# Optimization experiments

Measured on AMD Instinct MI355X. Metric: run time of the kernel, lower is better.

## Reference

```python
import jax, jax.numpy as jnp
import numpy as np

BETA = 0.9
TH = 1.0
SLOPE = 25.0  # fast-sigmoid surrogate slope (spike_grad_slope)

@jax.custom_vjp
def spike_fn(m):
    # Heaviside on (mem - threshold)
    return (m > 0).astype(m.dtype)

def _spike_fwd(m):
    return spike_fn(m), m

def _spike_bwd(m, g):
    # fast-sigmoid surrogate gradient: 1 / (slope*|m| + 1)^2
    return (g / (SLOPE * jnp.abs(m) + 1.0) ** 2,)

spike_fn.defvjp(_spike_fwd, _spike_bwd)


def setup_inputs() -> dict:
    key = jax.random.key(0)
    k1, k2, k3 = jax.random.split(key, 3)
    T, B, I, H, O = 128, 8192, 2, 256, 2
    x = jax.random.normal(k1, (T, B, I), dtype=jnp.float32)
    # xavier_uniform with gain=1: limit = sqrt(6/(fan_in+fan_out))
    lim1 = float(np.sqrt(6.0 / (I + H)))
    lim2 = float(np.sqrt(6.0 / (H + O)))
    W1 = jax.random.uniform(k2, (H, I), jnp.float32, -lim1, lim1)
    W2 = jax.random.uniform(k3, (O, H), jnp.float32, -lim2, lim2)
    return {"x": x, "W1": W1, "W2": W2}


def reference(x, W1, W2):
    # Precompute all per-step input currents in one GEMM: [T,B,H]
    cur = jnp.einsum('tbi,hi->tbh', x, W1)
    B, H = cur.shape[1], cur.shape[2]
    mem0 = jnp.zeros((B, H), cur.dtype)

    def step(mem, c):
        # snntorch Leaky (reset_mechanism='subtract'):
        # reset based on PREVIOUS mem's spike, then leaky integrate, then fire
        reset = spike_fn(mem - TH)
        mem_new = BETA * mem + c - reset * TH
        spk = spike_fn(mem_new - TH)
        # original code detaches mem between steps (1-step truncated BPTT)
        return jax.lax.stop_gradient(mem_new), spk

    _, spk_rec = jax.lax.scan(step, mem0, cur)  # spk_rec: [T,B,H]
    spk_avg = spk_rec[-10:].mean(0)             # [B,H]
    out = jnp.einsum('bh,oh->bo', spk_avg, W2)  # [B,O]
    return out
```

## Files before the change

### kernel.cpp

```cpp
#include <hip/hip_runtime.h>


#define T_STEPS 128
#define BATCH   8192
#define HID     256
#define TAIL    10
#define RH      8
#define NP      (RH/2)
#define LB      64
#define NWAVE   4
#define HG      8
#define NBG     (BATCH / LB)
#define PF      8

typedef float f32x2 __attribute__((ext_vector_type(2)));

#define PK_MUL(d, a, b) asm("v_pk_mul_f32 %0, %1, %2" : "=v"(d) : "v"(a), "v"(b))
#define PK_ADD(d, a, b) asm("v_pk_add_f32 %0, %1, %2" : "=v"(d) : "v"(a), "v"(b))

__global__ __launch_bounds__(256) void snn_scan(const float* __restrict__ x,
                                                const float* __restrict__ W1,
                                                const float* __restrict__ W2,
                                                float2* __restrict__ partial) {
    const int tid   = threadIdx.x;
    const int lane  = tid & 63;
    const int wave  = tid >> 6;
    const int bg    = blockIdx.x & (NBG - 1);
    const int hg    = blockIdx.x >> 7;
    const int b     = bg * LB + lane;
    const int hbase = hg * (NWAVE * RH) + wave * RH;

    f32x2 w0p[NP], w1p[NP];
#pragma unroll
    for (int p = 0; p < NP; ++p) {
        w0p[p].x = W1[2 * (hbase + 2 * p)];
        w0p[p].y = W1[2 * (hbase + 2 * p + 1)];
        w1p[p].x = W1[2 * (hbase + 2 * p) + 1];
        w1p[p].y = W1[2 * (hbase + 2 * p + 1) + 1];
    }

    const float2* xp = (const float2*)x;

    f32x2 mem[NP], spkn[NP], cnt[NP];
#pragma unroll
    for (int p = 0; p < NP; ++p) {
        mem[p]  = f32x2{0.0f, 0.0f};
        spkn[p] = f32x2{0.0f, 0.0f};
        cnt[p]  = f32x2{0.0f, 0.0f};
    }

    const f32x2 k09 = {0.9f, 0.9f};

#define LOADX(t) xp[(size_t)(t) * BATCH + b]

#define STEPP(p)                                              \
    {                                                         \
        f32x2 t0, t1, cc, m1, m2;                             \
        PK_MUL(t0, xaa, w0p[p]);                              \
        PK_MUL(t1, xcc, w1p[p]);                              \
        PK_ADD(cc, t0, t1);                                   \
        PK_MUL(m1, k09, mem[p]);                              \
        PK_ADD(m2, m1, cc);                                   \
        PK_ADD(mem[p], m2, spkn[p]);                          \
        spkn[p].x = (mem[p].x > 1.0f) ? -1.0f : 0.0f;         \
        spkn[p].y = (mem[p].y > 1.0f) ? -1.0f : 0.0f;         \
    }

    float2 buf[PF];
#pragma unroll
    for (int j = 0; j < PF; ++j) buf[j] = LOADX(j);

    for (int tb = 0; tb < T_STEPS - 2 * PF; tb += PF) {
#pragma unroll
        for (int j = 0; j < PF; ++j) {
            const float2 xv = buf[j];
            buf[j] = LOADX(tb + PF + j);
            const f32x2 xaa = {xv.x, xv.x};
            const f32x2 xcc = {xv.y, xv.y};
#pragma unroll
            for (int p = 0; p < NP; ++p) STEPP(p)
        }
    }

#pragma unroll
    for (int j = 0; j < PF; ++j) {
        const float2 xv = buf[j];
        buf[j] = LOADX(T_STEPS - PF + j);
        const f32x2 xaa = {xv.x, xv.x};
        const f32x2 xcc = {xv.y, xv.y};
#pragma unroll
        for (int p = 0; p < NP; ++p) {
            STEPP(p)
            if (j >= PF - 2) PK_ADD(cnt[p], cnt[p], spkn[p]);
        }
    }
#pragma unroll
    for (int j = 0; j < PF; ++j) {
        const float2 xv = buf[j];
        const f32x2 xaa = {xv.x, xv.x};
        const f32x2 xcc = {xv.y, xv.y};
#pragma unroll
        for (int p = 0; p < NP; ++p) {
            STEPP(p)
            PK_ADD(cnt[p], cnt[p], spkn[p]);
        }
    }
#undef STEPP
#undef LOADX

    float p0 = 0.0f, p1 = 0.0f;
#pragma unroll
    for (int p = 0; p < NP; ++p) {
        const float a0 = cnt[p].x / -10.0f;
        p0 = __fadd_rn(p0, __fmul_rn(a0, W2[hbase + 2 * p]));
        p1 = __fadd_rn(p1, __fmul_rn(a0, W2[HID + hbase + 2 * p]));
        const float a1 = cnt[p].y / -10.0f;
        p0 = __fadd_rn(p0, __fmul_rn(a1, W2[hbase + 2 * p + 1]));
        p1 = __fadd_rn(p1, __fmul_rn(a1, W2[HID + hbase + 2 * p + 1]));
    }

    __shared__ float2 red[NWAVE][LB];
    red[wave][lane] = make_float2(p0, p1);
    __syncthreads();
    if (wave == 0) {
        const float2 a0 = red[0][lane], a1 = red[1][lane];
        const float2 a2 = red[2][lane], a3 = red[3][lane];
        float2 s;
        s.x = __fadd_rn(__fadd_rn(a0.x, a1.x), __fadd_rn(a2.x, a3.x));
        s.y = __fadd_rn(__fadd_rn(a0.y, a1.y), __fadd_rn(a2.y, a3.y));
        partial[(size_t)hg * BATCH + b] = s;
    }
}

__global__ __launch_bounds__(256) void snn_reduce(const float2* __restrict__ partial,
                                                  float2* __restrict__ out) {
    const int b = blockIdx.x * 256 + threadIdx.x;
    float sx = 0.0f, sy = 0.0f;
#pragma unroll
    for (int hg = 0; hg < HG; ++hg) {
        const float2 p = partial[(size_t)hg * BATCH + b];
        sx = __fadd_rn(sx, p.x);
        sy = __fadd_rn(sy, p.y);
    }
    out[b] = make_float2(sx, sy);
}

extern "C" void kernel_launch(void* const* d_in, const int* in_sizes, int n_in,
                              void* d_out, int out_size, void* d_ws, size_t ws_size,
                              hipStream_t stream) {
    const float* x  = (const float*)d_in[0];
    const float* W1 = (const float*)d_in[1];
    const float* W2 = (const float*)d_in[2];
    float2* out     = (float2*)d_out;
    float2* partial = (float2*)d_ws;

    snn_scan<<<NBG * HG, 256, 0, stream>>>(x, W1, W2, partial);
    snn_reduce<<<BATCH / 256, 256, 0, stream>>>(partial, out);
}
```

Baseline: 103.0 us.

## Fuse cross-block reduction into scan kernel and restructure input-current packed math

Removes the separate reduce kernel launch. The last block of each batch group to finish, detected by a global atomic counter, sums the partials and writes the output. The counter is reset afterwards. Separately, the per-step current computation now multiplies the raw (x0,x1) pair by packed (w0,w1) weights and adds the halves with scalar adds, instead of broadcasting x components. This drops the broadcast moves but changes the instruction mix, and it adds fences and an atomic per block.

```diff
diff --git a/kernel.cpp b/kernel.cpp
--- a/kernel.cpp
+++ b/kernel.cpp
@@ -18,10 +18,13 @@
 #define PK_MUL(d, a, b) asm("v_pk_mul_f32 %0, %1, %2" : "=v"(d) : "v"(a), "v"(b))
 #define PK_ADD(d, a, b) asm("v_pk_add_f32 %0, %1, %2" : "=v"(d) : "v"(a), "v"(b))
 
+__device__ unsigned int bg_done[NBG];
+
 __global__ __launch_bounds__(256) void snn_scan(const float* __restrict__ x,
                                                 const float* __restrict__ W1,
                                                 const float* __restrict__ W2,
-                                                float2* __restrict__ partial) {
+                                                float2* __restrict__ partial,
+                                                float2* __restrict__ out) {
     const int tid   = threadIdx.x;
     const int lane  = tid & 63;
     const int wave  = tid >> 6;
@@ -30,16 +33,12 @@
     const int b     = bg * LB + lane;
     const int hbase = hg * (NWAVE * RH) + wave * RH;
 
-    f32x2 w0p[NP], w1p[NP];
+    f32x2 w01[RH];
+    const f32x2* w1v = (const f32x2*)W1;
 #pragma unroll
-    for (int p = 0; p < NP; ++p) {
-        w0p[p].x = W1[2 * (hbase + 2 * p)];
-        w0p[p].y = W1[2 * (hbase + 2 * p + 1)];
-        w1p[p].x = W1[2 * (hbase + 2 * p) + 1];
-        w1p[p].y = W1[2 * (hbase + 2 * p + 1) + 1];
-    }
+    for (int r = 0; r < RH; ++r) w01[r] = w1v[hbase + r];
 
-    const float2* xp = (const float2*)x;
+    const f32x2* xp = (const f32x2*)x;
 
     f32x2 mem[NP], spkn[NP], cnt[NP];
 #pragma unroll
@@ -53,30 +52,29 @@
 
 #define LOADX(t) xp[(size_t)(t) * BATCH + b]
 
-#define STEPP(p)                                              \
-    {                                                         \
-        f32x2 t0, t1, cc, m1, m2;                             \
-        PK_MUL(t0, xaa, w0p[p]);                              \
-        PK_MUL(t1, xcc, w1p[p]);                              \
-        PK_ADD(cc, t0, t1);                                   \
-        PK_MUL(m1, k09, mem[p]);                              \
-        PK_ADD(m2, m1, cc);                                   \
-        PK_ADD(mem[p], m2, spkn[p]);                          \
-        spkn[p].x = (mem[p].x > 1.0f) ? -1.0f : 0.0f;         \
-        spkn[p].y = (mem[p].y > 1.0f) ? -1.0f : 0.0f;         \
+#define STEPP(p)                                                      \
+    {                                                                 \
+        f32x2 te, to, cc, m1, m2;                                     \
+        PK_MUL(te, xv, w01[2 * (p)]);                                 \
+        PK_MUL(to, xv, w01[2 * (p) + 1]);                             \
+        cc.x = __fadd_rn(te.x, te.y);                                 \
+        cc.y = __fadd_rn(to.x, to.y);                                 \
+        PK_MUL(m1, k09, mem[p]);                                      \
+        PK_ADD(m2, m1, cc);                                           \
+        PK_ADD(mem[p], m2, spkn[p]);                                  \
+        spkn[p].x = (mem[p].x > 1.0f) ? -1.0f : 0.0f;                 \
+        spkn[p].y = (mem[p].y > 1.0f) ? -1.0f : 0.0f;                 \
     }
 
-    float2 buf[PF];
+    f32x2 buf[PF];
 #pragma unroll
     for (int j = 0; j < PF; ++j) buf[j] = LOADX(j);
 
     for (int tb = 0; tb < T_STEPS - 2 * PF; tb += PF) {
 #pragma unroll
         for (int j = 0; j < PF; ++j) {
-            const float2 xv = buf[j];
+            const f32x2 xv = buf[j];
             buf[j] = LOADX(tb + PF + j);
-            const f32x2 xaa = {xv.x, xv.x};
-            const f32x2 xcc = {xv.y, xv.y};
 #pragma unroll
             for (int p = 0; p < NP; ++p) STEPP(p)
         }
@@ -84,10 +82,8 @@
 
 #pragma unroll
     for (int j = 0; j < PF; ++j) {
-        const float2 xv = buf[j];
+        const f32x2 xv = buf[j];
         buf[j] = LOADX(T_STEPS - PF + j);
-        const f32x2 xaa = {xv.x, xv.x};
-        const f32x2 xcc = {xv.y, xv.y};
 #pragma unroll
         for (int p = 0; p < NP; ++p) {
             STEPP(p)
@@ -96,9 +92,7 @@
     }
 #pragma unroll
     for (int j = 0; j < PF; ++j) {
-        const float2 xv = buf[j];
-        const f32x2 xaa = {xv.x, xv.x};
-        const f32x2 xcc = {xv.y, xv.y};
+        const f32x2 xv = buf[j];
 #pragma unroll
         for (int p = 0; p < NP; ++p) {
             STEPP(p)
@@ -129,20 +123,25 @@
         s.x = __fadd_rn(__fadd_rn(a0.x, a1.x), __fadd_rn(a2.x, a3.x));
         s.y = __fadd_rn(__fadd_rn(a0.y, a1.y), __fadd_rn(a2.y, a3.y));
         partial[(size_t)hg * BATCH + b] = s;
+
+        __threadfence();
+        unsigned int old = 0;
+        if (lane == 0) old = atomicAdd(&bg_done[bg], 1u);
+        old = (unsigned int)__shfl((int)old, 0);
+
+        if (old == HG - 1) {
+            __threadfence();
+            float sx = 0.0f, sy = 0.0f;
+#pragma unroll
+            for (int hgi = 0; hgi < HG; ++hgi) {
+                const float2 pv = partial[(size_t)hgi * BATCH + b];
+                sx = __fadd_rn(sx, pv.x);
+                sy = __fadd_rn(sy, pv.y);
+            }
+            out[b] = make_float2(sx, sy);
+            if (lane == 0) bg_done[bg] = 0u;
+        }
     }
-}
-
-__global__ __launch_bounds__(256) void snn_reduce(const float2* __restrict__ partial,
-                                                  float2* __restrict__ out) {
-    const int b = blockIdx.x * 256 + threadIdx.x;
-    float sx = 0.0f, sy = 0.0f;
-#pragma unroll
-    for (int hg = 0; hg < HG; ++hg) {
-        const float2 p = partial[(size_t)hg * BATCH + b];
-        sx = __fadd_rn(sx, p.x);
-        sy = __fadd_rn(sy, p.y);
-    }
-    out[b] = make_float2(sx, sy);
 }
 
 extern "C" void kernel_launch(void* const* d_in, const int* in_sizes, int n_in,
@@ -154,6 +153,5 @@
     float2* out     = (float2*)d_out;
     float2* partial = (float2*)d_ws;
 
-    snn_scan<<<NBG * HG, 256, 0, stream>>>(x, W1, W2, partial);
-    snn_reduce<<<BATCH / 256, 256, 0, stream>>>(partial, out);
+    snn_scan<<<NBG * HG, 256, 0, stream>>>(x, W1, W2, partial, out);
 }
```

New measurement: 124.0 us. +20.4%, slower.
